# Kernel optimization log

Hardware: AMD Instinct MI355X
Metric: run time of the kernel (lower is better)

Reference implementation:

```python
import jax, jax.numpy as jnp
import numpy as np

NUM_HEADS = 4
LN_EPS = 1e-5


def setup_inputs() -> dict:
    key = jax.random.key(0)
    ks = jax.random.split(key, 5)
    C = 256
    x = jax.random.normal(ks[0], (2, C, 64, 64), dtype=jnp.float32)
    in_proj_w = jax.random.normal(ks[1], (3 * C, C), dtype=jnp.float32) * (1.0 / np.sqrt(C))
    in_proj_b = jax.random.normal(ks[2], (3 * C,), dtype=jnp.float32) * 0.02
    out_w = jax.random.normal(ks[3], (C, C), dtype=jnp.float32) * (1.0 / np.sqrt(C))
    out_b = jax.random.normal(ks[4], (C,), dtype=jnp.float32) * 0.02
    ln_g = jnp.ones((C,), dtype=jnp.float32)
    ln_b = jnp.zeros((C,), dtype=jnp.float32)
    return {"x": x, "in_proj_w": in_proj_w, "in_proj_b": in_proj_b,
            "out_w": out_w, "out_b": out_b, "ln_g": ln_g, "ln_b": ln_b}


def reference(x, in_proj_w, in_proj_b, out_w, out_b, ln_g, ln_b):
    b, c, H, W = x.shape
    S = H * W  # 4096 == max_tokens -> no pooling, no interpolation
    hd = c // NUM_HEADS
    t = x.reshape(b, c, S).transpose(0, 2, 1)  # (b, S, c)
    # fused QKV projection (in_proj_weight is [3c, c], rows = q,k,v blocks)
    qkv = t @ in_proj_w.T + in_proj_b  # (b, S, 3c)
    q, k, v = jnp.split(qkv, 3, axis=-1)
    def to_heads(a):
        return a.reshape(b, S, NUM_HEADS, hd).transpose(0, 2, 1, 3)  # (b, h, S, d)
    q = to_heads(q) * (1.0 / np.sqrt(hd))
    k = to_heads(k)
    v = to_heads(v)
    scores = jnp.einsum('bhqd,bhkd->bhqk', q, k)      # (b, h, S, S)
    probs = jax.nn.softmax(scores, axis=-1)
    attn = jnp.einsum('bhqk,bhkd->bhqd', probs, v)    # (b, h, S, d)
    attn = attn.transpose(0, 2, 1, 3).reshape(b, S, c)
    out = attn @ out_w.T + out_b                      # output projection
    # LayerNorm over channel dim
    mu = jnp.mean(out, axis=-1, keepdims=True)
    var = jnp.mean(jnp.square(out - mu), axis=-1, keepdims=True)
    out = (out - mu) * jax.lax.rsqrt(var + LN_EPS) * ln_g + ln_b
    return out.transpose(0, 2, 1).reshape(b, c, H, W)
```

## Files before the change

kernel.cpp:

```cpp
#include <hip/hip_runtime.h>
#include <cstddef>

#define S_TOK 4096
#define CDIM 256
#define NHEADS 4
#define HDIM 64
#define LSK 72
#define LDA 36
#define LDY 264
#define LOG2E 1.44269504f

typedef __attribute__((ext_vector_type(8))) short short8;
typedef __attribute__((ext_vector_type(4))) float floatx4;

__device__ inline unsigned short f2bf(float f) {
  union { float f; unsigned u; } v;
  v.f = f;
  unsigned r = v.u + 0x7fff + ((v.u >> 16) & 1);
  return (unsigned short)(r >> 16);
}
__device__ inline float bf2f(unsigned short u) {
  union { unsigned u; float f; } v;
  v.u = ((unsigned)u) << 16;
  return v.f;
}
__device__ inline unsigned pack_bf16(float a, float b) {
#if __has_builtin(__builtin_amdgcn_cvt_pk_bf16_f32)
  typedef __bf16 bf16x2 __attribute__((ext_vector_type(2)));
  union { bf16x2 v; unsigned u; } r;
  r.v = __builtin_amdgcn_cvt_pk_bf16_f32(a, b);
  return r.u;
#else
  return ((unsigned)f2bf(b) << 16) | f2bf(a);
#endif
}

__global__ __launch_bounds__(256) void qkv_gemm_kernel(
    const float* __restrict__ x, const float* __restrict__ ipw,
    const float* __restrict__ ipb, unsigned short* __restrict__ q16,
    unsigned short* __restrict__ k16, unsigned short* __restrict__ vt16) {
  __shared__ __align__(16) unsigned short As[64 * LDA];
  __shared__ __align__(16) unsigned short Bs[3][64 * LDA];
  const int tid = threadIdx.x;
  const int wave = tid >> 6, lane = tid & 63;
  const int quad = lane >> 4, l16 = lane & 15;
  const int n0 = blockIdx.x * 64;
  const int tok0 = blockIdx.y * 64;
  const int b = blockIdx.z;

  const int c_l = tid >> 3, t8 = tid & 7;
  const float* gx = x + (((size_t)(b * CDIM + c_l)) << 12) + tok0 + t8 * 8;
  unsigned short* wa = &As[(t8 * 8) * LDA + c_l];

  const int rr = tid >> 2, c4 = tid & 3;
  const float* gw0 = ipw + ((size_t)(n0 + rr)) * CDIM + c4 * 8;
  unsigned short* wb0 = &Bs[0][rr * LDA + c4 * 8];

  floatx4 acc[3][4];
#pragma unroll
  for (int s = 0; s < 3; ++s)
#pragma unroll
    for (int nt = 0; nt < 4; ++nt) acc[s][nt] = (floatx4){0.f, 0.f, 0.f, 0.f};

  float4 a0 = *(const float4*)(gx);
  float4 a1 = *(const float4*)(gx + 4);
  float4 bp[3][2];
#pragma unroll
  for (int s = 0; s < 3; ++s) {
    bp[s][0] = *(const float4*)(gw0 + (size_t)s * 256 * CDIM);
    bp[s][1] = *(const float4*)(gw0 + (size_t)s * 256 * CDIM + 4);
  }

  for (int ks = 0; ks < 8; ++ks) {
    __syncthreads();
    {
      unsigned p;
      p = pack_bf16(a0.x, a0.y);
      wa[0 * LDA] = (unsigned short)p; wa[1 * LDA] = (unsigned short)(p >> 16);
      p = pack_bf16(a0.z, a0.w);
      wa[2 * LDA] = (unsigned short)p; wa[3 * LDA] = (unsigned short)(p >> 16);
      p = pack_bf16(a1.x, a1.y);
      wa[4 * LDA] = (unsigned short)p; wa[5 * LDA] = (unsigned short)(p >> 16);
      p = pack_bf16(a1.z, a1.w);
      wa[6 * LDA] = (unsigned short)p; wa[7 * LDA] = (unsigned short)(p >> 16);
    }
#pragma unroll
    for (int s = 0; s < 3; ++s) {
      uint2 u0, u1;
      u0.x = pack_bf16(bp[s][0].x, bp[s][0].y);
      u0.y = pack_bf16(bp[s][0].z, bp[s][0].w);
      u1.x = pack_bf16(bp[s][1].x, bp[s][1].y);
      u1.y = pack_bf16(bp[s][1].z, bp[s][1].w);
      unsigned short* w = wb0 + s * 64 * LDA;
      *(uint2*)w = u0;
      *(uint2*)(w + 4) = u1;
    }
    __syncthreads();
    if (ks < 7) {
      const float* gxn = gx + ((size_t)((ks + 1) * 32) << 12);
      a0 = *(const float4*)(gxn);
      a1 = *(const float4*)(gxn + 4);
#pragma unroll
      for (int s = 0; s < 3; ++s) {
        const float* g = gw0 + (size_t)s * 256 * CDIM + (ks + 1) * 32;
        bp[s][0] = *(const float4*)(g);
        bp[s][1] = *(const float4*)(g + 4);
      }
    }
    short8 af = *(const short8*)&As[(wave * 16 + l16) * LDA + quad * 8];
#pragma unroll
    for (int s = 0; s < 3; ++s)
#pragma unroll
      for (int nt = 0; nt < 4; ++nt) {
        short8 bf = *(const short8*)&Bs[s][(nt * 16 + l16) * LDA + quad * 8];
        acc[s][nt] = __builtin_amdgcn_mfma_f32_16x16x32_bf16(af, bf, acc[s][nt], 0, 0, 0);
      }
  }

  const float qsc = 0.125f * LOG2E;
#pragma unroll
  for (int nt = 0; nt < 4; ++nt) {
    int cb = n0 + nt * 16 + l16;
    int h = cb >> 6, dh = cb & 63;
    float bq = ipb[cb], bk = ipb[256 + cb], bv = ipb[512 + cb];
    size_t base = ((size_t)(b * NHEADS + h)) * S_TOK;
#pragma unroll
    for (int r = 0; r < 4; ++r) {
      int tok = tok0 + wave * 16 + quad * 4 + r;
      q16[(base + tok) * HDIM + dh] = f2bf((acc[0][nt][r] + bq) * qsc);
      k16[(base + tok) * HDIM + dh] = f2bf(acc[1][nt][r] + bk);
    }
    int tokv = tok0 + wave * 16 + quad * 4;
    uint2 u;
    u.x = pack_bf16(acc[2][nt][0] + bv, acc[2][nt][1] + bv);
    u.y = pack_bf16(acc[2][nt][2] + bv, acc[2][nt][3] + bv);
    *(uint2*)&vt16[(base * 0 + ((size_t)(b * NHEADS + h) * HDIM + dh)) * S_TOK + tokv] = u;
  }
}

__global__ __launch_bounds__(256) void attn_kernel(
    const unsigned short* __restrict__ q16,
    const unsigned short* __restrict__ k16,
    const unsigned short* __restrict__ vt16,
    unsigned short* __restrict__ op, float* __restrict__ lp) {
  __shared__ __align__(16) unsigned short Ks[64 * LSK];
  __shared__ __align__(16) unsigned short Vt[64 * LSK];
  __shared__ __align__(16) unsigned short Ps[4 * 64 * LSK];

  const int tid = threadIdx.x;
  const int wave = tid >> 6;
  const int lane = tid & 63;
  const int quad = lane >> 4;
  const int l16 = lane & 15;
  const int bh = blockIdx.y;
  const int q0 = blockIdx.x * 256;
  const int split = blockIdx.z;
  const int kt0 = split * 16;

  short8 qf[4][2];
#pragma unroll
  for (int mt = 0; mt < 4; ++mt) {
    const unsigned short* qg =
        q16 + ((size_t)bh * S_TOK + q0 + wave * 64 + mt * 16 + l16) * HDIM + quad * 8;
    qf[mt][0] = *(const short8*)(qg);
    qf[mt][1] = *(const short8*)(qg + 32);
  }

  const int sr = tid >> 3, scc = tid & 7;
  const unsigned short* kg = k16 + ((size_t)bh * S_TOK + sr) * HDIM + scc * 8;
  const unsigned short* vg = vt16 + ((size_t)bh * HDIM + sr) * S_TOK + scc * 8;
  unsigned short* ksw = &Ks[sr * LSK + scc * 8];
  unsigned short* vtw = &Vt[sr * LSK + scc * 8];

  floatx4 O[4][4];
  float lsum[4] = {0.f, 0.f, 0.f, 0.f};
#pragma unroll
  for (int mt = 0; mt < 4; ++mt)
#pragma unroll
    for (int nt = 0; nt < 4; ++nt) O[mt][nt] = (floatx4){0.f, 0.f, 0.f, 0.f};

  uint4 k0r = *(const uint4*)(kg + (size_t)kt0 * 64 * HDIM);
  uint4 k1r = *(const uint4*)(kg + (size_t)kt0 * 64 * HDIM + 32 * HDIM);
  uint4 v0r = *(const uint4*)(vg + kt0 * 64);
  uint4 v1r = *(const uint4*)(vg + kt0 * 64 + (size_t)32 * S_TOK);

  unsigned short* pw = &Ps[(wave * 64) * LSK];

  for (int t = 0; t < 16; ++t) {
    __syncthreads();
    *(uint4*)ksw = k0r;
    *(uint4*)(ksw + 32 * LSK) = k1r;
    *(uint4*)vtw = v0r;
    *(uint4*)(vtw + 32 * LSK) = v1r;
    __syncthreads();
    if (t < 15) {
      const unsigned short* kgn = kg + (size_t)(kt0 + t + 1) * 64 * HDIM;
      const unsigned short* vgn = vg + (kt0 + t + 1) * 64;
      k0r = *(const uint4*)(kgn);
      k1r = *(const uint4*)(kgn + 32 * HDIM);
      v0r = *(const uint4*)(vgn);
      v1r = *(const uint4*)(vgn + (size_t)32 * S_TOK);
    }

#pragma unroll
    for (int kt = 0; kt < 4; ++kt) {
      short8 kf0 = *(const short8*)(&Ks[(kt * 16 + l16) * LSK + quad * 8]);
      short8 kf1 = *(const short8*)(&Ks[(kt * 16 + l16) * LSK + 32 + quad * 8]);
#pragma unroll
      for (int mt = 0; mt < 4; ++mt) {
        floatx4 c = (floatx4){0.f, 0.f, 0.f, 0.f};
        c = __builtin_amdgcn_mfma_f32_16x16x32_bf16(kf0, qf[mt][0], c, 0, 0, 0);
        c = __builtin_amdgcn_mfma_f32_16x16x32_bf16(kf1, qf[mt][1], c, 0, 0, 0);
        float p0 = __builtin_amdgcn_exp2f(c[0]);
        float p1 = __builtin_amdgcn_exp2f(c[1]);
        float p2 = __builtin_amdgcn_exp2f(c[2]);
        float p3 = __builtin_amdgcn_exp2f(c[3]);
        lsum[mt] += (p0 + p1) + (p2 + p3);
        uint2 pk;
        pk.x = pack_bf16(p0, p1);
        pk.y = pack_bf16(p2, p3);
        *(uint2*)&pw[(mt * 16 + l16) * LSK + kt * 16 + quad * 4] = pk;
      }
    }

    short8 pf[4][2];
#pragma unroll
    for (int mt = 0; mt < 4; ++mt) {
      pf[mt][0] = *(const short8*)(&pw[(mt * 16 + l16) * LSK + quad * 8]);
      pf[mt][1] = *(const short8*)(&pw[(mt * 16 + l16) * LSK + 32 + quad * 8]);
    }
#pragma unroll
    for (int nt = 0; nt < 4; ++nt) {
      short8 vf0 = *(const short8*)(&Vt[(nt * 16 + l16) * LSK + quad * 8]);
      short8 vf1 = *(const short8*)(&Vt[(nt * 16 + l16) * LSK + 32 + quad * 8]);
#pragma unroll
      for (int mt = 0; mt < 4; ++mt) {
        O[mt][nt] = __builtin_amdgcn_mfma_f32_16x16x32_bf16(pf[mt][0], vf0, O[mt][nt], 0, 0, 0);
        O[mt][nt] = __builtin_amdgcn_mfma_f32_16x16x32_bf16(pf[mt][1], vf1, O[mt][nt], 0, 0, 0);
      }
    }
  }

  const int b = bh >> 2, h = bh & 3;
  unsigned short* op_s = op + (size_t)split * 2097152;
  float* lp_s = lp + (size_t)split * 32768;
#pragma unroll
  for (int mt = 0; mt < 4; ++mt) {
    float ls = lsum[mt];
    ls += __shfl_xor(ls, 16);
    ls += __shfl_xor(ls, 32);
    if (quad == 0)
      lp_s[bh * S_TOK + q0 + wave * 64 + mt * 16 + l16] = ls;
#pragma unroll
    for (int r = 0; r < 4; ++r) {
      int row = q0 + wave * 64 + mt * 16 + quad * 4 + r;
#pragma unroll
      for (int nt = 0; nt < 4; ++nt)
        op_s[((size_t)(b * S_TOK + row)) * CDIM + h * HDIM + nt * 16 + l16] =
            f2bf(O[mt][nt][r]);
    }
  }
}

__device__ inline uint2 merge4(const unsigned short* op, size_t off, float rinv) {
  float s0 = 0.f, s1 = 0.f, s2 = 0.f, s3 = 0.f;
#pragma unroll
  for (int sp = 0; sp < 4; ++sp) {
    uint2 u = *(const uint2*)(op + (size_t)sp * 2097152 + off);
    s0 += bf2f((unsigned short)(u.x & 0xffff));
    s1 += bf2f((unsigned short)(u.x >> 16));
    s2 += bf2f((unsigned short)(u.y & 0xffff));
    s3 += bf2f((unsigned short)(u.y >> 16));
  }
  uint2 r;
  r.x = pack_bf16(s0 * rinv, s1 * rinv);
  r.y = pack_bf16(s2 * rinv, s3 * rinv);
  return r;
}

__global__ __launch_bounds__(256) void out_ln_gemm_kernel(
    const unsigned short* __restrict__ op, const float* __restrict__ lp,
    const float* __restrict__ ow, const float* __restrict__ obias,
    const float* __restrict__ lng, const float* __restrict__ lnb,
    float* __restrict__ out) {
  __shared__ __align__(16) unsigned short As[32 * LDA];
  __shared__ __align__(16) unsigned short Bs[256 * LDA];
  __shared__ __align__(16) float ys[32 * LDY];
  __shared__ float rsum[128];
  const int tid = threadIdx.x;
  const int wave = tid >> 6, lane = tid & 63;
  const int quad = lane >> 4, l16 = lane & 15;
  const int tok0 = blockIdx.x * 32;

  if (tid < 128) {
    int t = tid >> 2, h = tid & 3;
    int bb = tok0 >> 12;
    int idx = (bb * 4 + h) * 4096 + (tok0 & 4095) + t;
    rsum[tid] =
        1.0f / (lp[idx] + lp[32768 + idx] + lp[65536 + idx] + lp[98304 + idx]);
  }
  __syncthreads();

  const int ar = tid >> 3, ac = tid & 7;
  const size_t abase = (size_t)(tok0 + ar) * CDIM + ac * 4;
  unsigned short* wAp = &As[ar * LDA + ac * 4];
  const int rr = tid >> 2, c4 = tid & 3;
  const float* gB = ow + (size_t)rr * CDIM + c4 * 8;
  unsigned short* wBp = &Bs[rr * LDA + c4 * 8];

  floatx4 acc[2][4];
#pragma unroll
  for (int mt = 0; mt < 2; ++mt)
#pragma unroll
    for (int nt = 0; nt < 4; ++nt) acc[mt][nt] = (floatx4){0.f, 0.f, 0.f, 0.f};

  uint2 ap = merge4(op, abase, rsum[(ar << 2) + (ac >> 4)]);
  float4 bpf[4][2];
#pragma unroll
  for (int i = 0; i < 4; ++i) {
    bpf[i][0] = *(const float4*)(gB + (size_t)i * 64 * CDIM);
    bpf[i][1] = *(const float4*)(gB + (size_t)i * 64 * CDIM + 4);
  }

  for (int ks = 0; ks < 8; ++ks) {
    __syncthreads();
    *(uint2*)wAp = ap;
#pragma unroll
    for (int i = 0; i < 4; ++i) {
      uint2 u0, u1;
      u0.x = pack_bf16(bpf[i][0].x, bpf[i][0].y);
      u0.y = pack_bf16(bpf[i][0].z, bpf[i][0].w);
      u1.x = pack_bf16(bpf[i][1].x, bpf[i][1].y);
      u1.y = pack_bf16(bpf[i][1].z, bpf[i][1].w);
      unsigned short* w = wBp + i * 64 * LDA;
      *(uint2*)w = u0;
      *(uint2*)(w + 4) = u1;
    }
    __syncthreads();
    if (ks < 7) {
      int off = (ks + 1) * 32;
      int ch = off + ac * 4;
      ap = merge4(op, abase + off, rsum[(ar << 2) + (ch >> 6)]);
#pragma unroll
      for (int i = 0; i < 4; ++i) {
        bpf[i][0] = *(const float4*)(gB + (size_t)i * 64 * CDIM + off);
        bpf[i][1] = *(const float4*)(gB + (size_t)i * 64 * CDIM + off + 4);
      }
    }
    short8 af[2], bf[4];
#pragma unroll
    for (int mt = 0; mt < 2; ++mt)
      af[mt] = *(const short8*)&As[(mt * 16 + l16) * LDA + quad * 8];
#pragma unroll
    for (int nt = 0; nt < 4; ++nt)
      bf[nt] = *(const short8*)&Bs[(wave * 64 + nt * 16 + l16) * LDA + quad * 8];
#pragma unroll
    for (int mt = 0; mt < 2; ++mt)
#pragma unroll
      for (int nt = 0; nt < 4; ++nt)
        acc[mt][nt] = __builtin_amdgcn_mfma_f32_16x16x32_bf16(af[mt], bf[nt], acc[mt][nt], 0, 0, 0);
  }

#pragma unroll
  for (int mt = 0; mt < 2; ++mt)
#pragma unroll
    for (int nt = 0; nt < 4; ++nt) {
      int c = wave * 64 + nt * 16 + l16;
      float bo = obias[c];
#pragma unroll
      for (int r = 0; r < 4; ++r)
        ys[(mt * 16 + quad * 4 + r) * LDY + c] = acc[mt][nt][r] + bo;
    }
  __syncthreads();

  const int gtok = tid >> 3, l8 = tid & 7;
  float sum = 0.f, ssq = 0.f;
#pragma unroll
  for (int i = 0; i < 32; ++i) {
    float v = ys[gtok * LDY + i * 8 + l8];
    sum += v;
    ssq += v * v;
  }
  sum += __shfl_xor(sum, 1); ssq += __shfl_xor(ssq, 1);
  sum += __shfl_xor(sum, 2); ssq += __shfl_xor(ssq, 2);
  sum += __shfl_xor(sum, 4); ssq += __shfl_xor(ssq, 4);
  float mu = sum * (1.f / 256.f);
  float var = ssq * (1.f / 256.f) - mu * mu;
  float rstd = rsqrtf(var + 1e-5f);
  const int b2 = tok0 >> 12;
  const int sl = (tok0 & 4095) + gtok;
#pragma unroll
  for (int i = 0; i < 32; ++i) {
    int c = i * 8 + l8;
    float v = ys[gtok * LDY + c];
    out[(((size_t)(b2 * CDIM + c)) << 12) + sl] = (v - mu) * rstd * lng[c] + lnb[c];
  }
}

extern "C" void kernel_launch(void* const* d_in, const int* in_sizes, int n_in,
                              void* d_out, int out_size, void* d_ws, size_t ws_size,
                              hipStream_t stream) {
  const float* x = (const float*)d_in[0];
  const float* ipw = (const float*)d_in[1];
  const float* ipb = (const float*)d_in[2];
  const float* ow = (const float*)d_in[3];
  const float* ob = (const float*)d_in[4];
  const float* lng = (const float*)d_in[5];
  const float* lnb = (const float*)d_in[6];
  float* out = (float*)d_out;
  unsigned short* q16 = (unsigned short*)d_ws;
  unsigned short* k16 = q16 + 2097152;
  unsigned short* vt16 = k16 + 2097152;
  unsigned short* op = vt16 + 2097152;
  float* lp = (float*)(op + 8388608);

  qkv_gemm_kernel<<<dim3(4, 64, 2), 256, 0, stream>>>(x, ipw, ipb, q16, k16, vt16);
  attn_kernel<<<dim3(16, 8, 4), 256, 0, stream>>>(q16, k16, vt16, op, lp);
  out_ln_gemm_kernel<<<256, 256, 0, stream>>>(op, lp, ow, ob, lng, lnb, out);
}
```

Before: 149.6 us.

## Halve out-projection token tile and coalesce transposed LayerNorm output stores

```diff
diff --git a/kernel.cpp b/kernel.cpp
--- a/kernel.cpp
+++ b/kernel.cpp
@@ -7,7 +7,7 @@
 #define HDIM 64
 #define LSK 72
 #define LDA 36
-#define LDY 264
+#define LDY 257
 #define LOG2E 1.44269504f
 
 typedef __attribute__((ext_vector_type(8))) short short8;
@@ -51,7 +51,6 @@
   const int c_l = tid >> 3, t8 = tid & 7;
   const float* gx = x + (((size_t)(b * CDIM + c_l)) << 12) + tok0 + t8 * 8;
   unsigned short* wa = &As[(t8 * 8) * LDA + c_l];
-
   const int rr = tid >> 2, c4 = tid & 3;
   const float* gw0 = ipw + ((size_t)(n0 + rr)) * CDIM + c4 * 8;
   unsigned short* wb0 = &Bs[0][rr * LDA + c4 * 8];
@@ -134,7 +133,7 @@
     uint2 u;
     u.x = pack_bf16(acc[2][nt][0] + bv, acc[2][nt][1] + bv);
     u.y = pack_bf16(acc[2][nt][2] + bv, acc[2][nt][3] + bv);
-    *(uint2*)&vt16[(base * 0 + ((size_t)(b * NHEADS + h) * HDIM + dh)) * S_TOK + tokv] = u;
+    *(uint2*)&vt16[((size_t)(b * NHEADS + h) * HDIM + dh) * S_TOK + tokv] = u;
   }
 }
 
@@ -262,20 +261,15 @@
   }
 }
 
-__device__ inline uint2 merge4(const unsigned short* op, size_t off, float rinv) {
-  float s0 = 0.f, s1 = 0.f, s2 = 0.f, s3 = 0.f;
+__device__ inline unsigned merge2(const unsigned short* op, size_t off, float rinv) {
+  float lo = 0.f, hi = 0.f;
 #pragma unroll
   for (int sp = 0; sp < 4; ++sp) {
-    uint2 u = *(const uint2*)(op + (size_t)sp * 2097152 + off);
-    s0 += bf2f((unsigned short)(u.x & 0xffff));
-    s1 += bf2f((unsigned short)(u.x >> 16));
-    s2 += bf2f((unsigned short)(u.y & 0xffff));
-    s3 += bf2f((unsigned short)(u.y >> 16));
-  }
-  uint2 r;
-  r.x = pack_bf16(s0 * rinv, s1 * rinv);
-  r.y = pack_bf16(s2 * rinv, s3 * rinv);
-  return r;
+    unsigned u = *(const unsigned*)(op + (size_t)sp * 2097152 + off);
+    lo += bf2f((unsigned short)(u & 0xffff));
+    hi += bf2f((unsigned short)(u >> 16));
+  }
+  return pack_bf16(lo * rinv, hi * rinv);
 }
 
 __global__ __launch_bounds__(256) void out_ln_gemm_kernel(
@@ -283,38 +277,38 @@
     const float* __restrict__ ow, const float* __restrict__ obias,
     const float* __restrict__ lng, const float* __restrict__ lnb,
     float* __restrict__ out) {
-  __shared__ __align__(16) unsigned short As[32 * LDA];
+  __shared__ __align__(16) unsigned short As[16 * LDA];
   __shared__ __align__(16) unsigned short Bs[256 * LDA];
-  __shared__ __align__(16) float ys[32 * LDY];
-  __shared__ float rsum[128];
+  __shared__ __align__(16) float ys[16 * LDY];
+  __shared__ float rsum[64];
+  __shared__ float mu_s[16], rs_s[16];
   const int tid = threadIdx.x;
   const int wave = tid >> 6, lane = tid & 63;
   const int quad = lane >> 4, l16 = lane & 15;
-  const int tok0 = blockIdx.x * 32;
-
-  if (tid < 128) {
+  const int tok0 = blockIdx.x * 16;
+  const int bb = tok0 >> 12;
+  const int sbase = tok0 & 4095;
+
+  if (tid < 64) {
     int t = tid >> 2, h = tid & 3;
-    int bb = tok0 >> 12;
-    int idx = (bb * 4 + h) * 4096 + (tok0 & 4095) + t;
+    int idx = (bb * 4 + h) * 4096 + sbase + t;
     rsum[tid] =
         1.0f / (lp[idx] + lp[32768 + idx] + lp[65536 + idx] + lp[98304 + idx]);
   }
   __syncthreads();
 
-  const int ar = tid >> 3, ac = tid & 7;
-  const size_t abase = (size_t)(tok0 + ar) * CDIM + ac * 4;
-  unsigned short* wAp = &As[ar * LDA + ac * 4];
+  const int ar = tid >> 4, ac = tid & 15;
+  const size_t abase = (size_t)(tok0 + ar) * CDIM + ac * 2;
+  unsigned short* wAp = &As[ar * LDA + ac * 2];
   const int rr = tid >> 2, c4 = tid & 3;
   const float* gB = ow + (size_t)rr * CDIM + c4 * 8;
   unsigned short* wBp = &Bs[rr * LDA + c4 * 8];
 
-  floatx4 acc[2][4];
-#pragma unroll
-  for (int mt = 0; mt < 2; ++mt)
-#pragma unroll
-    for (int nt = 0; nt < 4; ++nt) acc[mt][nt] = (floatx4){0.f, 0.f, 0.f, 0.f};
-
-  uint2 ap = merge4(op, abase, rsum[(ar << 2) + (ac >> 4)]);
+  floatx4 acc[4];
+#pragma unroll
+  for (int nt = 0; nt < 4; ++nt) acc[nt] = (floatx4){0.f, 0.f, 0.f, 0.f};
+
+  unsigned ap = merge2(op, abase, rsum[ar * 4]);
   float4 bpf[4][2];
 #pragma unroll
   for (int i = 0; i < 4; ++i) {
@@ -324,7 +318,7 @@
 
   for (int ks = 0; ks < 8; ++ks) {
     __syncthreads();
-    *(uint2*)wAp = ap;
+    *(unsigned*)wAp = ap;
 #pragma unroll
     for (int i = 0; i < 4; ++i) {
       uint2 u0, u1;
@@ -339,61 +333,59 @@
     __syncthreads();
     if (ks < 7) {
       int off = (ks + 1) * 32;
-      int ch = off + ac * 4;
-      ap = merge4(op, abase + off, rsum[(ar << 2) + (ch >> 6)]);
+      ap = merge2(op, abase + off, rsum[ar * 4 + ((ks + 1) >> 1)]);
 #pragma unroll
       for (int i = 0; i < 4; ++i) {
         bpf[i][0] = *(const float4*)(gB + (size_t)i * 64 * CDIM + off);
         bpf[i][1] = *(const float4*)(gB + (size_t)i * 64 * CDIM + off + 4);
       }
     }
-    short8 af[2], bf[4];
-#pragma unroll
-    for (int mt = 0; mt < 2; ++mt)
-      af[mt] = *(const short8*)&As[(mt * 16 + l16) * LDA + quad * 8];
-#pragma unroll
-    for (int nt = 0; nt < 4; ++nt)
-      bf[nt] = *(const short8*)&Bs[(wave * 64 + nt * 16 + l16) * LDA + quad * 8];
-#pragma unroll
-    for (int mt = 0; mt < 2; ++mt)
-#pragma unroll
-      for (int nt = 0; nt < 4; ++nt)
-        acc[mt][nt] = __builtin_amdgcn_mfma_f32_16x16x32_bf16(af[mt], bf[nt], acc[mt][nt], 0, 0, 0);
-  }
-
-#pragma unroll
-  for (int mt = 0; mt < 2; ++mt)
+    short8 af = *(const short8*)&As[l16 * LDA + quad * 8];
 #pragma unroll
     for (int nt = 0; nt < 4; ++nt) {
-      int c = wave * 64 + nt * 16 + l16;
-      float bo = obias[c];
-#pragma unroll
-      for (int r = 0; r < 4; ++r)
-        ys[(mt * 16 + quad * 4 + r) * LDY + c] = acc[mt][nt][r] + bo;
-    }
+      short8 bf = *(const short8*)&Bs[(wave * 64 + nt * 16 + l16) * LDA + quad * 8];
+      acc[nt] = __builtin_amdgcn_mfma_f32_16x16x32_bf16(af, bf, acc[nt], 0, 0, 0);
+    }
+  }
+
+#pragma unroll
+  for (int nt = 0; nt < 4; ++nt) {
+    int c = wave * 64 + nt * 16 + l16;
+    float bo = obias[c];
+#pragma unroll
+    for (int r = 0; r < 4; ++r)
+      ys[(quad * 4 + r) * LDY + c] = acc[nt][r] + bo;
+  }
   __syncthreads();
 
-  const int gtok = tid >> 3, l8 = tid & 7;
+  const int gtok = tid >> 4, lx = tid & 15;
   float sum = 0.f, ssq = 0.f;
 #pragma unroll
-  for (int i = 0; i < 32; ++i) {
-    float v = ys[gtok * LDY + i * 8 + l8];
+  for (int i = 0; i < 16; ++i) {
+    float v = ys[gtok * LDY + i * 16 + lx];
     sum += v;
     ssq += v * v;
   }
   sum += __shfl_xor(sum, 1); ssq += __shfl_xor(ssq, 1);
   sum += __shfl_xor(sum, 2); ssq += __shfl_xor(ssq, 2);
   sum += __shfl_xor(sum, 4); ssq += __shfl_xor(ssq, 4);
+  sum += __shfl_xor(sum, 8); ssq += __shfl_xor(ssq, 8);
   float mu = sum * (1.f / 256.f);
   float var = ssq * (1.f / 256.f) - mu * mu;
   float rstd = rsqrtf(var + 1e-5f);
-  const int b2 = tok0 >> 12;
-  const int sl = (tok0 & 4095) + gtok;
-#pragma unroll
-  for (int i = 0; i < 32; ++i) {
-    int c = i * 8 + l8;
-    float v = ys[gtok * LDY + c];
-    out[(((size_t)(b2 * CDIM + c)) << 12) + sl] = (v - mu) * rstd * lng[c] + lnb[c];
+  if (lx == 0) {
+    mu_s[gtok] = mu;
+    rs_s[gtok] = rstd;
+  }
+  __syncthreads();
+
+#pragma unroll
+  for (int i = 0; i < 16; ++i) {
+    int flat = i * 256 + tid;
+    int t = flat & 15, c = flat >> 4;
+    float v = ys[t * LDY + c];
+    out[(((size_t)(bb * CDIM + c)) << 12) + sbase + t] =
+        (v - mu_s[t]) * rs_s[t] * lng[c] + lnb[c];
   }
 }
 
@@ -416,5 +408,5 @@
 
   qkv_gemm_kernel<<<dim3(4, 64, 2), 256, 0, stream>>>(x, ipw, ipb, q16, k16, vt16);
   attn_kernel<<<dim3(16, 8, 4), 256, 0, stream>>>(q16, k16, vt16, op, lp);
-  out_ln_gemm_kernel<<<256, 256, 0, stream>>>(op, lp, ow, ob, lng, lnb, out);
-}
+  out_ln_gemm_kernel<<<512, 256, 0, stream>>>(op, lp, ow, ob, lng, lnb, out);
+}
```

Result: slower. 157.0 us (+5.0%).

## Fuse QKV, attention and output-LN kernels into one persistent kernel with grid barriers

Applied to the files above, without the earlier changes.

```diff
diff --git a/kernel.cpp b/kernel.cpp
--- a/kernel.cpp
+++ b/kernel.cpp
@@ -7,8 +7,9 @@
 #define HDIM 64
 #define LSK 72
 #define LDA 36
-#define LDY 264
+#define LDY 257
 #define LOG2E 1.44269504f
+#define NBLK 512u
 
 typedef __attribute__((ext_vector_type(8))) short short8;
 typedef __attribute__((ext_vector_type(4))) float floatx4;
@@ -33,233 +34,6 @@
 #else
   return ((unsigned)f2bf(b) << 16) | f2bf(a);
 #endif
-}
-
-__global__ __launch_bounds__(256) void qkv_gemm_kernel(
-    const float* __restrict__ x, const float* __restrict__ ipw,
-    const float* __restrict__ ipb, unsigned short* __restrict__ q16,
-    unsigned short* __restrict__ k16, unsigned short* __restrict__ vt16) {
-  __shared__ __align__(16) unsigned short As[64 * LDA];
-  __shared__ __align__(16) unsigned short Bs[3][64 * LDA];
-  const int tid = threadIdx.x;
-  const int wave = tid >> 6, lane = tid & 63;
-  const int quad = lane >> 4, l16 = lane & 15;
-  const int n0 = blockIdx.x * 64;
-  const int tok0 = blockIdx.y * 64;
-  const int b = blockIdx.z;
-
-  const int c_l = tid >> 3, t8 = tid & 7;
-  const float* gx = x + (((size_t)(b * CDIM + c_l)) << 12) + tok0 + t8 * 8;
-  unsigned short* wa = &As[(t8 * 8) * LDA + c_l];
-
-  const int rr = tid >> 2, c4 = tid & 3;
-  const float* gw0 = ipw + ((size_t)(n0 + rr)) * CDIM + c4 * 8;
-  unsigned short* wb0 = &Bs[0][rr * LDA + c4 * 8];
-
-  floatx4 acc[3][4];
-#pragma unroll
-  for (int s = 0; s < 3; ++s)
-#pragma unroll
-    for (int nt = 0; nt < 4; ++nt) acc[s][nt] = (floatx4){0.f, 0.f, 0.f, 0.f};
-
-  float4 a0 = *(const float4*)(gx);
-  float4 a1 = *(const float4*)(gx + 4);
-  float4 bp[3][2];
-#pragma unroll
-  for (int s = 0; s < 3; ++s) {
-    bp[s][0] = *(const float4*)(gw0 + (size_t)s * 256 * CDIM);
-    bp[s][1] = *(const float4*)(gw0 + (size_t)s * 256 * CDIM + 4);
-  }
-
-  for (int ks = 0; ks < 8; ++ks) {
-    __syncthreads();
-    {
-      unsigned p;
-      p = pack_bf16(a0.x, a0.y);
-      wa[0 * LDA] = (unsigned short)p; wa[1 * LDA] = (unsigned short)(p >> 16);
-      p = pack_bf16(a0.z, a0.w);
-      wa[2 * LDA] = (unsigned short)p; wa[3 * LDA] = (unsigned short)(p >> 16);
-      p = pack_bf16(a1.x, a1.y);
-      wa[4 * LDA] = (unsigned short)p; wa[5 * LDA] = (unsigned short)(p >> 16);
-      p = pack_bf16(a1.z, a1.w);
-      wa[6 * LDA] = (unsigned short)p; wa[7 * LDA] = (unsigned short)(p >> 16);
-    }
-#pragma unroll
-    for (int s = 0; s < 3; ++s) {
-      uint2 u0, u1;
-      u0.x = pack_bf16(bp[s][0].x, bp[s][0].y);
-      u0.y = pack_bf16(bp[s][0].z, bp[s][0].w);
-      u1.x = pack_bf16(bp[s][1].x, bp[s][1].y);
-      u1.y = pack_bf16(bp[s][1].z, bp[s][1].w);
-      unsigned short* w = wb0 + s * 64 * LDA;
-      *(uint2*)w = u0;
-      *(uint2*)(w + 4) = u1;
-    }
-    __syncthreads();
-    if (ks < 7) {
-      const float* gxn = gx + ((size_t)((ks + 1) * 32) << 12);
-      a0 = *(const float4*)(gxn);
-      a1 = *(const float4*)(gxn + 4);
-#pragma unroll
-      for (int s = 0; s < 3; ++s) {
-        const float* g = gw0 + (size_t)s * 256 * CDIM + (ks + 1) * 32;
-        bp[s][0] = *(const float4*)(g);
-        bp[s][1] = *(const float4*)(g + 4);
-      }
-    }
-    short8 af = *(const short8*)&As[(wave * 16 + l16) * LDA + quad * 8];
-#pragma unroll
-    for (int s = 0; s < 3; ++s)
-#pragma unroll
-      for (int nt = 0; nt < 4; ++nt) {
-        short8 bf = *(const short8*)&Bs[s][(nt * 16 + l16) * LDA + quad * 8];
-        acc[s][nt] = __builtin_amdgcn_mfma_f32_16x16x32_bf16(af, bf, acc[s][nt], 0, 0, 0);
-      }
-  }
-
-  const float qsc = 0.125f * LOG2E;
-#pragma unroll
-  for (int nt = 0; nt < 4; ++nt) {
-    int cb = n0 + nt * 16 + l16;
-    int h = cb >> 6, dh = cb & 63;
-    float bq = ipb[cb], bk = ipb[256 + cb], bv = ipb[512 + cb];
-    size_t base = ((size_t)(b * NHEADS + h)) * S_TOK;
-#pragma unroll
-    for (int r = 0; r < 4; ++r) {
-      int tok = tok0 + wave * 16 + quad * 4 + r;
-      q16[(base + tok) * HDIM + dh] = f2bf((acc[0][nt][r] + bq) * qsc);
-      k16[(base + tok) * HDIM + dh] = f2bf(acc[1][nt][r] + bk);
-    }
-    int tokv = tok0 + wave * 16 + quad * 4;
-    uint2 u;
-    u.x = pack_bf16(acc[2][nt][0] + bv, acc[2][nt][1] + bv);
-    u.y = pack_bf16(acc[2][nt][2] + bv, acc[2][nt][3] + bv);
-    *(uint2*)&vt16[(base * 0 + ((size_t)(b * NHEADS + h) * HDIM + dh)) * S_TOK + tokv] = u;
-  }
-}
-
-__global__ __launch_bounds__(256) void attn_kernel(
-    const unsigned short* __restrict__ q16,
-    const unsigned short* __restrict__ k16,
-    const unsigned short* __restrict__ vt16,
-    unsigned short* __restrict__ op, float* __restrict__ lp) {
-  __shared__ __align__(16) unsigned short Ks[64 * LSK];
-  __shared__ __align__(16) unsigned short Vt[64 * LSK];
-  __shared__ __align__(16) unsigned short Ps[4 * 64 * LSK];
-
-  const int tid = threadIdx.x;
-  const int wave = tid >> 6;
-  const int lane = tid & 63;
-  const int quad = lane >> 4;
-  const int l16 = lane & 15;
-  const int bh = blockIdx.y;
-  const int q0 = blockIdx.x * 256;
-  const int split = blockIdx.z;
-  const int kt0 = split * 16;
-
-  short8 qf[4][2];
-#pragma unroll
-  for (int mt = 0; mt < 4; ++mt) {
-    const unsigned short* qg =
-        q16 + ((size_t)bh * S_TOK + q0 + wave * 64 + mt * 16 + l16) * HDIM + quad * 8;
-    qf[mt][0] = *(const short8*)(qg);
-    qf[mt][1] = *(const short8*)(qg + 32);
-  }
-
-  const int sr = tid >> 3, scc = tid & 7;
-  const unsigned short* kg = k16 + ((size_t)bh * S_TOK + sr) * HDIM + scc * 8;
-  const unsigned short* vg = vt16 + ((size_t)bh * HDIM + sr) * S_TOK + scc * 8;
-  unsigned short* ksw = &Ks[sr * LSK + scc * 8];
-  unsigned short* vtw = &Vt[sr * LSK + scc * 8];
-
-  floatx4 O[4][4];
-  float lsum[4] = {0.f, 0.f, 0.f, 0.f};
-#pragma unroll
-  for (int mt = 0; mt < 4; ++mt)
-#pragma unroll
-    for (int nt = 0; nt < 4; ++nt) O[mt][nt] = (floatx4){0.f, 0.f, 0.f, 0.f};
-
-  uint4 k0r = *(const uint4*)(kg + (size_t)kt0 * 64 * HDIM);
-  uint4 k1r = *(const uint4*)(kg + (size_t)kt0 * 64 * HDIM + 32 * HDIM);
-  uint4 v0r = *(const uint4*)(vg + kt0 * 64);
-  uint4 v1r = *(const uint4*)(vg + kt0 * 64 + (size_t)32 * S_TOK);
-
-  unsigned short* pw = &Ps[(wave * 64) * LSK];
-
-  for (int t = 0; t < 16; ++t) {
-    __syncthreads();
-    *(uint4*)ksw = k0r;
-    *(uint4*)(ksw + 32 * LSK) = k1r;
-    *(uint4*)vtw = v0r;
-    *(uint4*)(vtw + 32 * LSK) = v1r;
-    __syncthreads();
-    if (t < 15) {
-      const unsigned short* kgn = kg + (size_t)(kt0 + t + 1) * 64 * HDIM;
-      const unsigned short* vgn = vg + (kt0 + t + 1) * 64;
-      k0r = *(const uint4*)(kgn);
-      k1r = *(const uint4*)(kgn + 32 * HDIM);
-      v0r = *(const uint4*)(vgn);
-      v1r = *(const uint4*)(vgn + (size_t)32 * S_TOK);
-    }
-
-#pragma unroll
-    for (int kt = 0; kt < 4; ++kt) {
-      short8 kf0 = *(const short8*)(&Ks[(kt * 16 + l16) * LSK + quad * 8]);
-      short8 kf1 = *(const short8*)(&Ks[(kt * 16 + l16) * LSK + 32 + quad * 8]);
-#pragma unroll
-      for (int mt = 0; mt < 4; ++mt) {
-        floatx4 c = (floatx4){0.f, 0.f, 0.f, 0.f};
-        c = __builtin_amdgcn_mfma_f32_16x16x32_bf16(kf0, qf[mt][0], c, 0, 0, 0);
-        c = __builtin_amdgcn_mfma_f32_16x16x32_bf16(kf1, qf[mt][1], c, 0, 0, 0);
-        float p0 = __builtin_amdgcn_exp2f(c[0]);
-        float p1 = __builtin_amdgcn_exp2f(c[1]);
-        float p2 = __builtin_amdgcn_exp2f(c[2]);
-        float p3 = __builtin_amdgcn_exp2f(c[3]);
-        lsum[mt] += (p0 + p1) + (p2 + p3);
-        uint2 pk;
-        pk.x = pack_bf16(p0, p1);
-        pk.y = pack_bf16(p2, p3);
-        *(uint2*)&pw[(mt * 16 + l16) * LSK + kt * 16 + quad * 4] = pk;
-      }
-    }
-
-    short8 pf[4][2];
-#pragma unroll
-    for (int mt = 0; mt < 4; ++mt) {
-      pf[mt][0] = *(const short8*)(&pw[(mt * 16 + l16) * LSK + quad * 8]);
-      pf[mt][1] = *(const short8*)(&pw[(mt * 16 + l16) * LSK + 32 + quad * 8]);
-    }
-#pragma unroll
-    for (int nt = 0; nt < 4; ++nt) {
-      short8 vf0 = *(const short8*)(&Vt[(nt * 16 + l16) * LSK + quad * 8]);
-      short8 vf1 = *(const short8*)(&Vt[(nt * 16 + l16) * LSK + 32 + quad * 8]);
-#pragma unroll
-      for (int mt = 0; mt < 4; ++mt) {
-        O[mt][nt] = __builtin_amdgcn_mfma_f32_16x16x32_bf16(pf[mt][0], vf0, O[mt][nt], 0, 0, 0);
-        O[mt][nt] = __builtin_amdgcn_mfma_f32_16x16x32_bf16(pf[mt][1], vf1, O[mt][nt], 0, 0, 0);
-      }
-    }
-  }
-
-  const int b = bh >> 2, h = bh & 3;
-  unsigned short* op_s = op + (size_t)split * 2097152;
-  float* lp_s = lp + (size_t)split * 32768;
-#pragma unroll
-  for (int mt = 0; mt < 4; ++mt) {
-    float ls = lsum[mt];
-    ls += __shfl_xor(ls, 16);
-    ls += __shfl_xor(ls, 32);
-    if (quad == 0)
-      lp_s[bh * S_TOK + q0 + wave * 64 + mt * 16 + l16] = ls;
-#pragma unroll
-    for (int r = 0; r < 4; ++r) {
-      int row = q0 + wave * 64 + mt * 16 + quad * 4 + r;
-#pragma unroll
-      for (int nt = 0; nt < 4; ++nt)
-        op_s[((size_t)(b * S_TOK + row)) * CDIM + h * HDIM + nt * 16 + l16] =
-            f2bf(O[mt][nt][r]);
-    }
-  }
 }
 
 __device__ inline uint2 merge4(const unsigned short* op, size_t off, float rinv) {
@@ -278,122 +52,372 @@
   return r;
 }
 
-__global__ __launch_bounds__(256) void out_ln_gemm_kernel(
-    const unsigned short* __restrict__ op, const float* __restrict__ lp,
-    const float* __restrict__ ow, const float* __restrict__ obias,
-    const float* __restrict__ lng, const float* __restrict__ lnb,
-    float* __restrict__ out) {
-  __shared__ __align__(16) unsigned short As[32 * LDA];
-  __shared__ __align__(16) unsigned short Bs[256 * LDA];
-  __shared__ __align__(16) float ys[32 * LDY];
-  __shared__ float rsum[128];
+__device__ inline void grid_barrier(unsigned* cnt, unsigned target) {
+  __syncthreads();
+  __threadfence();
+  if (threadIdx.x == 0) {
+    __hip_atomic_fetch_add(cnt, 1u, __ATOMIC_ACQ_REL, __HIP_MEMORY_SCOPE_AGENT);
+    while (__hip_atomic_load(cnt, __ATOMIC_ACQUIRE, __HIP_MEMORY_SCOPE_AGENT) < target)
+      __builtin_amdgcn_s_sleep(8);
+  }
+  __syncthreads();
+  __threadfence();
+}
+
+union __align__(16) SharedMem {
+  struct {
+    unsigned short Ks[64 * LSK];
+    unsigned short Vt[64 * LSK];
+    unsigned short Ps[4 * 64 * LSK];
+  } a;
+  struct {
+    unsigned short As[64 * LDA];
+    unsigned short Bs[3][64 * LDA];
+  } q;
+  struct {
+    unsigned short As[32 * LDA];
+    unsigned short Bs[256 * LDA];
+    float ys[32 * LDY];
+    float rsum[128];
+    float mu_s[32], rs_s[32];
+  } o;
+};
+
+__global__ __launch_bounds__(256, 2) void mega_kernel(
+    const float* __restrict__ x, const float* __restrict__ ipw,
+    const float* __restrict__ ipb, const float* __restrict__ ow,
+    const float* __restrict__ obias, const float* __restrict__ lng,
+    const float* __restrict__ lnb, float* __restrict__ out,
+    unsigned short* __restrict__ q16, unsigned short* __restrict__ k16,
+    unsigned short* __restrict__ vt16, unsigned short* __restrict__ op,
+    float* __restrict__ lp, unsigned* __restrict__ bar) {
+  __shared__ SharedMem sm;
   const int tid = threadIdx.x;
+  const int bx = blockIdx.x;
   const int wave = tid >> 6, lane = tid & 63;
   const int quad = lane >> 4, l16 = lane & 15;
-  const int tok0 = blockIdx.x * 32;
-
-  if (tid < 128) {
-    int t = tid >> 2, h = tid & 3;
-    int bb = tok0 >> 12;
-    int idx = (bb * 4 + h) * 4096 + (tok0 & 4095) + t;
-    rsum[tid] =
-        1.0f / (lp[idx] + lp[32768 + idx] + lp[65536 + idx] + lp[98304 + idx]);
+
+  {
+    const int n0 = (bx & 3) * 64;
+    const int tok0 = ((bx >> 2) & 63) * 64;
+    const int b = bx >> 8;
+
+    const int c_l = tid >> 3, t8 = tid & 7;
+    const float* gx = x + (((size_t)(b * CDIM + c_l)) << 12) + tok0 + t8 * 8;
+    unsigned short* wa = &sm.q.As[(t8 * 8) * LDA + c_l];
+    const int rr = tid >> 2, c4 = tid & 3;
+    const float* gw0 = ipw + ((size_t)(n0 + rr)) * CDIM + c4 * 8;
+    unsigned short* wb0 = &sm.q.Bs[0][rr * LDA + c4 * 8];
+
+    floatx4 acc[3][4];
+#pragma unroll
+    for (int s = 0; s < 3; ++s)
+#pragma unroll
+      for (int nt = 0; nt < 4; ++nt) acc[s][nt] = (floatx4){0.f, 0.f, 0.f, 0.f};
+
+    float4 a0 = *(const float4*)(gx);
+    float4 a1 = *(const float4*)(gx + 4);
+    float4 bp[3][2];
+#pragma unroll
+    for (int s = 0; s < 3; ++s) {
+      bp[s][0] = *(const float4*)(gw0 + (size_t)s * 256 * CDIM);
+      bp[s][1] = *(const float4*)(gw0 + (size_t)s * 256 * CDIM + 4);
+    }
+
+    for (int ks = 0; ks < 8; ++ks) {
+      __syncthreads();
+      {
+        unsigned p;
+        p = pack_bf16(a0.x, a0.y);
+        wa[0 * LDA] = (unsigned short)p; wa[1 * LDA] = (unsigned short)(p >> 16);
+        p = pack_bf16(a0.z, a0.w);
+        wa[2 * LDA] = (unsigned short)p; wa[3 * LDA] = (unsigned short)(p >> 16);
+        p = pack_bf16(a1.x, a1.y);
+        wa[4 * LDA] = (unsigned short)p; wa[5 * LDA] = (unsigned short)(p >> 16);
+        p = pack_bf16(a1.z, a1.w);
+        wa[6 * LDA] = (unsigned short)p; wa[7 * LDA] = (unsigned short)(p >> 16);
+      }
+#pragma unroll
+      for (int s = 0; s < 3; ++s) {
+        uint2 u0, u1;
+        u0.x = pack_bf16(bp[s][0].x, bp[s][0].y);
+        u0.y = pack_bf16(bp[s][0].z, bp[s][0].w);
+        u1.x = pack_bf16(bp[s][1].x, bp[s][1].y);
+        u1.y = pack_bf16(bp[s][1].z, bp[s][1].w);
+        unsigned short* w = wb0 + s * 64 * LDA;
+        *(uint2*)w = u0;
+        *(uint2*)(w + 4) = u1;
+      }
+      __syncthreads();
+      if (ks < 7) {
+        const float* gxn = gx + ((size_t)((ks + 1) * 32) << 12);
+        a0 = *(const float4*)(gxn);
+        a1 = *(const float4*)(gxn + 4);
+#pragma unroll
+        for (int s = 0; s < 3; ++s) {
+          const float* g = gw0 + (size_t)s * 256 * CDIM + (ks + 1) * 32;
+          bp[s][0] = *(const float4*)(g);
+          bp[s][1] = *(const float4*)(g + 4);
+        }
+      }
+      short8 af = *(const short8*)&sm.q.As[(wave * 16 + l16) * LDA + quad * 8];
+#pragma unroll
+      for (int s = 0; s < 3; ++s)
+#pragma unroll
+        for (int nt = 0; nt < 4; ++nt) {
+          short8 bf = *(const short8*)&sm.q.Bs[s][(nt * 16 + l16) * LDA + quad * 8];
+          acc[s][nt] = __builtin_amdgcn_mfma_f32_16x16x32_bf16(af, bf, acc[s][nt], 0, 0, 0);
+        }
+    }
+
+    const float qsc = 0.125f * LOG2E;
+#pragma unroll
+    for (int nt = 0; nt < 4; ++nt) {
+      int cb = n0 + nt * 16 + l16;
+      int h = cb >> 6, dh = cb & 63;
+      float bq = ipb[cb], bk = ipb[256 + cb], bv = ipb[512 + cb];
+      size_t base = ((size_t)(b * NHEADS + h)) * S_TOK;
+#pragma unroll
+      for (int r = 0; r < 4; ++r) {
+        int tok = tok0 + wave * 16 + quad * 4 + r;
+        q16[(base + tok) * HDIM + dh] = f2bf((acc[0][nt][r] + bq) * qsc);
+        k16[(base + tok) * HDIM + dh] = f2bf(acc[1][nt][r] + bk);
+      }
+      int tokv = tok0 + wave * 16 + quad * 4;
+      uint2 u;
+      u.x = pack_bf16(acc[2][nt][0] + bv, acc[2][nt][1] + bv);
+      u.y = pack_bf16(acc[2][nt][2] + bv, acc[2][nt][3] + bv);
+      *(uint2*)&vt16[((size_t)(b * NHEADS + h) * HDIM + dh) * S_TOK + tokv] = u;
+    }
   }
-  __syncthreads();
-
-  const int ar = tid >> 3, ac = tid & 7;
-  const size_t abase = (size_t)(tok0 + ar) * CDIM + ac * 4;
-  unsigned short* wAp = &As[ar * LDA + ac * 4];
-  const int rr = tid >> 2, c4 = tid & 3;
-  const float* gB = ow + (size_t)rr * CDIM + c4 * 8;
-  unsigned short* wBp = &Bs[rr * LDA + c4 * 8];
-
-  floatx4 acc[2][4];
-#pragma unroll
-  for (int mt = 0; mt < 2; ++mt)
-#pragma unroll
-    for (int nt = 0; nt < 4; ++nt) acc[mt][nt] = (floatx4){0.f, 0.f, 0.f, 0.f};
-
-  uint2 ap = merge4(op, abase, rsum[(ar << 2) + (ac >> 4)]);
-  float4 bpf[4][2];
-#pragma unroll
-  for (int i = 0; i < 4; ++i) {
-    bpf[i][0] = *(const float4*)(gB + (size_t)i * 64 * CDIM);
-    bpf[i][1] = *(const float4*)(gB + (size_t)i * 64 * CDIM + 4);
+
+  grid_barrier(bar, NBLK);
+
+  {
+    const int bh = (bx >> 4) & 7;
+    const int q0 = (bx & 15) * 256;
+    const int split = bx >> 7;
+    const int kt0 = split * 16;
+
+    short8 qf[4][2];
+#pragma unroll
+    for (int mt = 0; mt < 4; ++mt) {
+      const unsigned short* qg =
+          q16 + ((size_t)bh * S_TOK + q0 + wave * 64 + mt * 16 + l16) * HDIM + quad * 8;
+      qf[mt][0] = *(const short8*)(qg);
+      qf[mt][1] = *(const short8*)(qg + 32);
+    }
+
+    const int sr = tid >> 3, scc = tid & 7;
+    const unsigned short* kg = k16 + ((size_t)bh * S_TOK + sr) * HDIM + scc * 8;
+    const unsigned short* vg = vt16 + ((size_t)bh * HDIM + sr) * S_TOK + scc * 8;
+    unsigned short* ksw = &sm.a.Ks[sr * LSK + scc * 8];
+    unsigned short* vtw = &sm.a.Vt[sr * LSK + scc * 8];
+
+    floatx4 O[4][4];
+    float lsum[4] = {0.f, 0.f, 0.f, 0.f};
+#pragma unroll
+    for (int mt = 0; mt < 4; ++mt)
+#pragma unroll
+      for (int nt = 0; nt < 4; ++nt) O[mt][nt] = (floatx4){0.f, 0.f, 0.f, 0.f};
+
+    uint4 k0r = *(const uint4*)(kg + (size_t)kt0 * 64 * HDIM);
+    uint4 k1r = *(const uint4*)(kg + (size_t)kt0 * 64 * HDIM + 32 * HDIM);
+    uint4 v0r = *(const uint4*)(vg + kt0 * 64);
+    uint4 v1r = *(const uint4*)(vg + kt0 * 64 + (size_t)32 * S_TOK);
+
+    unsigned short* pw = &sm.a.Ps[(wave * 64) * LSK];
+
+    for (int t = 0; t < 16; ++t) {
+      __syncthreads();
+      *(uint4*)ksw = k0r;
+      *(uint4*)(ksw + 32 * LSK) = k1r;
+      *(uint4*)vtw = v0r;
+      *(uint4*)(vtw + 32 * LSK) = v1r;
+      __syncthreads();
+      if (t < 15) {
+        const unsigned short* kgn = kg + (size_t)(kt0 + t + 1) * 64 * HDIM;
+        const unsigned short* vgn = vg + (kt0 + t + 1) * 64;
+        k0r = *(const uint4*)(kgn);
+        k1r = *(const uint4*)(kgn + 32 * HDIM);
+        v0r = *(const uint4*)(vgn);
+        v1r = *(const uint4*)(vgn + (size_t)32 * S_TOK);
+      }
+
+#pragma unroll
+      for (int kt = 0; kt < 4; ++kt) {
+        short8 kf0 = *(const short8*)(&sm.a.Ks[(kt * 16 + l16) * LSK + quad * 8]);
+        short8 kf1 = *(const short8*)(&sm.a.Ks[(kt * 16 + l16) * LSK + 32 + quad * 8]);
+#pragma unroll
+        for (int mt = 0; mt < 4; ++mt) {
+          floatx4 c = (floatx4){0.f, 0.f, 0.f, 0.f};
+          c = __builtin_amdgcn_mfma_f32_16x16x32_bf16(kf0, qf[mt][0], c, 0, 0, 0);
+          c = __builtin_amdgcn_mfma_f32_16x16x32_bf16(kf1, qf[mt][1], c, 0, 0, 0);
+          float p0 = __builtin_amdgcn_exp2f(c[0]);
+          float p1 = __builtin_amdgcn_exp2f(c[1]);
+          float p2 = __builtin_amdgcn_exp2f(c[2]);
+          float p3 = __builtin_amdgcn_exp2f(c[3]);
+          lsum[mt] += (p0 + p1) + (p2 + p3);
+          uint2 pk;
+          pk.x = pack_bf16(p0, p1);
+          pk.y = pack_bf16(p2, p3);
+          *(uint2*)&pw[(mt * 16 + l16) * LSK + kt * 16 + quad * 4] = pk;
+        }
+      }
+
+      short8 pf[4][2];
+#pragma unroll
+      for (int mt = 0; mt < 4; ++mt) {
+        pf[mt][0] = *(const short8*)(&pw[(mt * 16 + l16) * LSK + quad * 8]);
+        pf[mt][1] = *(const short8*)(&pw[(mt * 16 + l16) * LSK + 32 + quad * 8]);
+      }
+#pragma unroll
+      for (int nt = 0; nt < 4; ++nt) {
+        short8 vf0 = *(const short8*)(&sm.a.Vt[(nt * 16 + l16) * LSK + quad * 8]);
+        short8 vf1 = *(const short8*)(&sm.a.Vt[(nt * 16 + l16) * LSK + 32 + quad * 8]);
+#pragma unroll
+        for (int mt = 0; mt < 4; ++mt) {
+          O[mt][nt] = __builtin_amdgcn_mfma_f32_16x16x32_bf16(pf[mt][0], vf0, O[mt][nt], 0, 0, 0);
+          O[mt][nt] = __builtin_amdgcn_mfma_f32_16x16x32_bf16(pf[mt][1], vf1, O[mt][nt], 0, 0, 0);
+        }
+      }
+    }
+
+    const int b = bh >> 2, h = bh & 3;
+    unsigned short* op_s = op + (size_t)split * 2097152;
+    float* lp_s = lp + (size_t)split * 32768;
+#pragma unroll
+    for (int mt = 0; mt < 4; ++mt) {
+      float ls = lsum[mt];
+      ls += __shfl_xor(ls, 16);
+      ls += __shfl_xor(ls, 32);
+      if (quad == 0)
+        lp_s[bh * S_TOK + q0 + wave * 64 + mt * 16 + l16] = ls;
+#pragma unroll
+      for (int r = 0; r < 4; ++r) {
+        int row = q0 + wave * 64 + mt * 16 + quad * 4 + r;
+#pragma unroll
+        for (int nt = 0; nt < 4; ++nt)
+          op_s[((size_t)(b * S_TOK + row)) * CDIM + h * HDIM + nt * 16 + l16] =
+              f2bf(O[mt][nt][r]);
+      }
+    }
   }
 
-  for (int ks = 0; ks < 8; ++ks) {
+  grid_barrier(bar + 1, NBLK);
+
+  if (bx < 256) {
+    const int tok0 = bx * 32;
+    const int bb = tok0 >> 12;
+    const int sbase = tok0 & 4095;
+
+    if (tid < 128) {
+      int t = tid >> 2, h = tid & 3;
+      int idx = (bb * 4 + h) * 4096 + sbase + t;
+      sm.o.rsum[tid] =
+          1.0f / (lp[idx] + lp[32768 + idx] + lp[65536 + idx] + lp[98304 + idx]);
+    }
     __syncthreads();
-    *(uint2*)wAp = ap;
+
+    const int ar = tid >> 3, ac = tid & 7;
+    const size_t abase = (size_t)(tok0 + ar) * CDIM + ac * 4;
+    unsigned short* wAp = &sm.o.As[ar * LDA + ac * 4];
+    const int rr = tid >> 2, c4 = tid & 3;
+    const float* gB = ow + (size_t)rr * CDIM + c4 * 8;
+    unsigned short* wBp = &sm.o.Bs[rr * LDA + c4 * 8];
+
+    floatx4 acc[2][4];
+#pragma unroll
+    for (int mt = 0; mt < 2; ++mt)
+#pragma unroll
+      for (int nt = 0; nt < 4; ++nt) acc[mt][nt] = (floatx4){0.f, 0.f, 0.f, 0.f};
+
+    uint2 ap = merge4(op, abase, sm.o.rsum[ar * 4]);
+    float4 bpf[4][2];
 #pragma unroll
     for (int i = 0; i < 4; ++i) {
-      uint2 u0, u1;
-      u0.x = pack_bf16(bpf[i][0].x, bpf[i][0].y);
-      u0.y = pack_bf16(bpf[i][0].z, bpf[i][0].w);
-      u1.x = pack_bf16(bpf[i][1].x, bpf[i][1].y);
-      u1.y = pack_bf16(bpf[i][1].z, bpf[i][1].w);
-      unsigned short* w = wBp + i * 64 * LDA;
-      *(uint2*)w = u0;
-      *(uint2*)(w + 4) = u1;
-    }
+      bpf[i][0] = *(const float4*)(gB + (size_t)i * 64 * CDIM);
+      bpf[i][1] = *(const float4*)(gB + (size_t)i * 64 * CDIM + 4);
+    }
+
+    for (int ks = 0; ks < 8; ++ks) {
+      __syncthreads();
+      *(uint2*)wAp = ap;
+#pragma unroll
+      for (int i = 0; i < 4; ++i) {
+        uint2 u0, u1;
+        u0.x = pack_bf16(bpf[i][0].x, bpf[i][0].y);
+        u0.y = pack_bf16(bpf[i][0].z, bpf[i][0].w);
+        u1.x = pack_bf16(bpf[i][1].x, bpf[i][1].y);
+        u1.y = pack_bf16(bpf[i][1].z, bpf[i][1].w);
+        unsigned short* w = wBp + i * 64 * LDA;
+        *(uint2*)w = u0;
+        *(uint2*)(w + 4) = u1;
+      }
+      __syncthreads();
+      if (ks < 7) {
+        int off = (ks + 1) * 32;
+        ap = merge4(op, abase + off, sm.o.rsum[ar * 4 + ((ks + 1) >> 1)]);
+#pragma unroll
+        for (int i = 0; i < 4; ++i) {
+          bpf[i][0] = *(const float4*)(gB + (size_t)i * 64 * CDIM + off);
+          bpf[i][1] = *(const float4*)(gB + (size_t)i * 64 * CDIM + off + 4);
+        }
+      }
+      short8 af[2], bf[4];
+#pragma unroll
+      for (int mt = 0; mt < 2; ++mt)
+        af[mt] = *(const short8*)&sm.o.As[(mt * 16 + l16) * LDA + quad * 8];
+#pragma unroll
+      for (int nt = 0; nt < 4; ++nt)
+        bf[nt] = *(const short8*)&sm.o.Bs[(wave * 64 + nt * 16 + l16) * LDA + quad * 8];
+#pragma unroll
+      for (int mt = 0; mt < 2; ++mt)
+#pragma unroll
+        for (int nt = 0; nt < 4; ++nt)
+          acc[mt][nt] = __builtin_amdgcn_mfma_f32_16x16x32_bf16(af[mt], bf[nt], acc[mt][nt], 0, 0, 0);
+    }
+
+#pragma unroll
+    for (int mt = 0; mt < 2; ++mt)
+#pragma unroll
+      for (int nt = 0; nt < 4; ++nt) {
+        int c = wave * 64 + nt * 16 + l16;
+        float bo = obias[c];
+#pragma unroll
+        for (int r = 0; r < 4; ++r)
+          sm.o.ys[(mt * 16 + quad * 4 + r) * LDY + c] = acc[mt][nt][r] + bo;
+      }
     __syncthreads();
-    if (ks < 7) {
-      int off = (ks + 1) * 32;
-      int ch = off + ac * 4;
-      ap = merge4(op, abase + off, rsum[(ar << 2) + (ch >> 6)]);
-#pragma unroll
-      for (int i = 0; i < 4; ++i) {
-        bpf[i][0] = *(const float4*)(gB + (size_t)i * 64 * CDIM + off);
-        bpf[i][1] = *(const float4*)(gB + (size_t)i * 64 * CDIM + off + 4);
-      }
-    }
-    short8 af[2], bf[4];
-#pragma unroll
-    for (int mt = 0; mt < 2; ++mt)
-      af[mt] = *(const short8*)&As[(mt * 16 + l16) * LDA + quad * 8];
-#pragma unroll
-    for (int nt = 0; nt < 4; ++nt)
-      bf[nt] = *(const short8*)&Bs[(wave * 64 + nt * 16 + l16) * LDA + quad * 8];
-#pragma unroll
-    for (int mt = 0; mt < 2; ++mt)
-#pragma unroll
-      for (int nt = 0; nt < 4; ++nt)
-        acc[mt][nt] = __builtin_amdgcn_mfma_f32_16x16x32_bf16(af[mt], bf[nt], acc[mt][nt], 0, 0, 0);
-  }
-
-#pragma unroll
-  for (int mt = 0; mt < 2; ++mt)
-#pragma unroll
-    for (int nt = 0; nt < 4; ++nt) {
-      int c = wave * 64 + nt * 16 + l16;
-      float bo = obias[c];
-#pragma unroll
-      for (int r = 0; r < 4; ++r)
-        ys[(mt * 16 + quad * 4 + r) * LDY + c] = acc[mt][nt][r] + bo;
-    }
-  __syncthreads();
-
-  const int gtok = tid >> 3, l8 = tid & 7;
-  float sum = 0.f, ssq = 0.f;
-#pragma unroll
-  for (int i = 0; i < 32; ++i) {
-    float v = ys[gtok * LDY + i * 8 + l8];
-    sum += v;
-    ssq += v * v;
-  }
-  sum += __shfl_xor(sum, 1); ssq += __shfl_xor(ssq, 1);
-  sum += __shfl_xor(sum, 2); ssq += __shfl_xor(ssq, 2);
-  sum += __shfl_xor(sum, 4); ssq += __shfl_xor(ssq, 4);
-  float mu = sum * (1.f / 256.f);
-  float var = ssq * (1.f / 256.f) - mu * mu;
-  float rstd = rsqrtf(var + 1e-5f);
-  const int b2 = tok0 >> 12;
-  const int sl = (tok0 & 4095) + gtok;
-#pragma unroll
-  for (int i = 0; i < 32; ++i) {
-    int c = i * 8 + l8;
-    float v = ys[gtok * LDY + c];
-    out[(((size_t)(b2 * CDIM + c)) << 12) + sl] = (v - mu) * rstd * lng[c] + lnb[c];
+
+    const int gtok = tid >> 3, l8 = tid & 7;
+    float sum = 0.f, ssq = 0.f;
+#pragma unroll
+    for (int i = 0; i < 32; ++i) {
+      float v = sm.o.ys[gtok * LDY + i * 8 + l8];
+      sum += v;
+      ssq += v * v;
+    }
+    sum += __shfl_xor(sum, 1); ssq += __shfl_xor(ssq, 1);
+    sum += __shfl_xor(sum, 2); ssq += __shfl_xor(ssq, 2);
+    sum += __shfl_xor(sum, 4); ssq += __shfl_xor(ssq, 4);
+    float mu = sum * (1.f / 256.f);
+    float var = ssq * (1.f / 256.f) - mu * mu;
+    float rstd = rsqrtf(var + 1e-5f);
+    if (l8 == 0) {
+      sm.o.mu_s[gtok] = mu;
+      sm.o.rs_s[gtok] = rstd;
+    }
+    __syncthreads();
+
+#pragma unroll
+    for (int i = 0; i < 32; ++i) {
+      int flat = i * 256 + tid;
+      int t = flat & 31, c = flat >> 5;
+      float v = sm.o.ys[t * LDY + c];
+      out[(((size_t)(bb * CDIM + c)) << 12) + sbase + t] =
+          (v - sm.o.mu_s[t]) * sm.o.rs_s[t] * lng[c] + lnb[c];
+    }
   }
 }
 
@@ -413,8 +437,9 @@
   unsigned short* vt16 = k16 + 2097152;
   unsigned short* op = vt16 + 2097152;
   float* lp = (float*)(op + 8388608);
-
-  qkv_gemm_kernel<<<dim3(4, 64, 2), 256, 0, stream>>>(x, ipw, ipb, q16, k16, vt16);
-  attn_kernel<<<dim3(16, 8, 4), 256, 0, stream>>>(q16, k16, vt16, op, lp);
-  out_ln_gemm_kernel<<<256, 256, 0, stream>>>(op, lp, ow, ob, lng, lnb, out);
-}
+  unsigned* bar = (unsigned*)(lp + 131072);
+
+  hipMemsetAsync(bar, 0, 2 * sizeof(unsigned), stream);
+  mega_kernel<<<dim3(NBLK), 256, 0, stream>>>(x, ipw, ipb, ow, ob, lng, lnb, out,
+                                              q16, k16, vt16, op, lp, bar);
+}
```

Result: slower. 428.3 us (+186.3%).
